# Optimization experiments

Measured on AMD Instinct MI355X. Metric: run time of the kernel, lower is better.

Reference implementation:

```python
import jax, jax.numpy as jnp
import numpy as np

B, N, D, H = 8, 1024, 768, 12
DH = D // H
DFF = 4 * D
EPS = 1e-5


def setup_inputs() -> dict:
    key = jax.random.key(0)
    ks = jax.random.split(key, 16)
    s = 0.02
    return {
        "x": jax.random.normal(ks[0], (B, N, D), jnp.float32),
        "ln1_g": jnp.ones((D,), jnp.float32),
        "ln1_b": jnp.zeros((D,), jnp.float32),
        "wqkv": jax.random.normal(ks[1], (D, 3 * D), jnp.float32) * s,
        "bqkv": jnp.zeros((3 * D,), jnp.float32),
        "wo": jax.random.normal(ks[2], (D, D), jnp.float32) * s,
        "bo": jnp.zeros((D,), jnp.float32),
        "rel_bias": jax.random.normal(ks[3], (H, N, N), jnp.float32) * s,
        "ln2_g": jnp.ones((D,), jnp.float32),
        "ln2_b": jnp.zeros((D,), jnp.float32),
        "w1": jax.random.normal(ks[4], (D, DFF), jnp.float32) * s,
        "b1": jnp.zeros((DFF,), jnp.float32),
        "w2": jax.random.normal(ks[5], (DFF, D), jnp.float32) * s,
        "b2": jnp.zeros((D,), jnp.float32),
    }


def _layer_norm(x, g, b):
    mu = jnp.mean(x, axis=-1, keepdims=True)
    var = jnp.mean(jnp.square(x - mu), axis=-1, keepdims=True)
    return (x - mu) * jax.lax.rsqrt(var + EPS) * g + b


def reference(x, ln1_g, ln1_b, wqkv, bqkv, wo, bo, rel_bias, ln2_g, ln2_b, w1, b1, w2, b2):
    # --- pre-norm self-attention with relative position bias + residual ---
    h = _layer_norm(x, ln1_g, ln1_b)
    qkv = h @ wqkv + bqkv                      # [B, N, 3D]
    qkv = qkv.reshape(B, N, 3, H, DH)
    q, k, v = qkv[:, :, 0], qkv[:, :, 1], qkv[:, :, 2]  # each [B, N, H, DH]
    scale = 1.0 / jnp.sqrt(jnp.asarray(DH, x.dtype))
    scores = jnp.einsum("bnhd,bmhd->bhnm", q, k) * scale + rel_bias[None]
    attn = jax.nn.softmax(scores, axis=-1)
    ctx = jnp.einsum("bhnm,bmhd->bnhd", attn, v).reshape(B, N, D)
    x = ctx @ wo + bo + x
    # --- pre-norm FFN (GELU) + residual ---
    h = _layer_norm(x, ln2_g, ln2_b)
    h = jax.nn.gelu(h @ w1 + b1)
    x = h @ w2 + b2 + x
    return x
```

## Files before the change

### kernel.cpp

```cpp
#include <hip/hip_runtime.h>
#include <hip/hip_bf16.h>
#include <math.h>

#define D_MODEL 768
#define NTOK    8192
#define SEQ     1024
#define NH      12
#define DHD     64
#define DFF     3072

typedef __attribute__((ext_vector_type(8)))  __bf16 bf16x8;
typedef __attribute__((ext_vector_type(4)))  float  f32x4;
typedef __attribute__((ext_vector_type(16))) float  f32x16;
typedef __attribute__((ext_vector_type(4)))  unsigned short us4;

typedef const __attribute__((address_space(1))) void g_void;
typedef __attribute__((address_space(3))) void lds_void;

__device__ __forceinline__ unsigned short f2bf(float f) {
  unsigned u = __float_as_uint(f);
  u += 0x7fffu + ((u >> 16) & 1u);
  return (unsigned short)(u >> 16);
}

__device__ __forceinline__ f32x4 mfma16(bf16x8 a, bf16x8 b, f32x4 c) {
  return __builtin_amdgcn_mfma_f32_16x16x32_bf16(a, b, c, 0, 0, 0);
}
__device__ __forceinline__ f32x16 mfma32(bf16x8 a, bf16x8 b, f32x16 c) {
  return __builtin_amdgcn_mfma_f32_32x32x16_bf16(a, b, c, 0, 0, 0);
}

__device__ __forceinline__ void gload_lds16(const unsigned short* g, unsigned short* l) {
  __builtin_amdgcn_global_load_lds((g_void*)g, (lds_void*)l, 16, 0, 0);
}

__global__ __launch_bounds__(256)
void ln_kernel(const float* __restrict__ x, const float* __restrict__ gam,
               const float* __restrict__ bet, unsigned short* __restrict__ out) {
  const int w = threadIdx.x >> 6, lane = threadIdx.x & 63;
  const size_t row = (size_t)blockIdx.x * 4 + w;
  const float* xr = x + row * D_MODEL;
  f32x4 v[3];
#pragma unroll
  for (int c = 0; c < 3; ++c) v[c] = *(const f32x4*)(xr + c * 256 + lane * 4);
  float s = 0.f;
#pragma unroll
  for (int c = 0; c < 3; ++c)
#pragma unroll
    for (int j = 0; j < 4; ++j) s += v[c][j];
#pragma unroll
  for (int o = 32; o; o >>= 1) s += __shfl_xor(s, o);
  const float mu = s * (1.0f / D_MODEL);
  float vs = 0.f;
#pragma unroll
  for (int c = 0; c < 3; ++c)
#pragma unroll
    for (int j = 0; j < 4; ++j) { float d = v[c][j] - mu; vs += d * d; }
#pragma unroll
  for (int o = 32; o; o >>= 1) vs += __shfl_xor(vs, o);
  const float rs = rsqrtf(vs * (1.0f / D_MODEL) + 1e-5f);
  unsigned short* orow = out + row * D_MODEL;
#pragma unroll
  for (int c = 0; c < 3; ++c) {
    us4 o4;
#pragma unroll
    for (int j = 0; j < 4; ++j) {
      int idx = c * 256 + lane * 4 + j;
      o4[j] = f2bf((v[c][j] - mu) * rs * gam[idx] + bet[idx]);
    }
    *(us4*)(orow + c * 256 + lane * 4) = o4;
  }
}

__global__ __launch_bounds__(256)
void wtrans_kernel(const float* __restrict__ W, unsigned short* __restrict__ Wt,
                   int K, int Nc) {
  __shared__ float t[32][33];
  const int tx = threadIdx.x & 31, ty = threadIdx.x >> 5;
  const int nb = blockIdx.x * 32, kb = blockIdx.y * 32;
#pragma unroll
  for (int i = 0; i < 4; ++i)
    t[ty + 8 * i][tx] = W[(size_t)(kb + ty + 8 * i) * Nc + nb + tx];
  __syncthreads();
#pragma unroll
  for (int i = 0; i < 4; ++i)
    Wt[(size_t)(nb + ty + 8 * i) * K + kb + tx] = f2bf(t[tx][ty + 8 * i]);
}

__global__ __launch_bounds__(256)
void brelayout_kernel(const float* __restrict__ rel, unsigned short* __restrict__ bF) {
  const int gw = blockIdx.x * 4 + (threadIdx.x >> 6);
  const int lane = threadIdx.x & 63;
  const int ktg = gw & 31, qt = (gw >> 5) & 31, h = gw >> 10;
  const int q = qt * 32 + (lane & 31), hi = lane >> 5;
  const float* src = rel + ((size_t)h * SEQ + q) * SEQ + ktg * 32 + 4 * hi;
  unsigned ow[8];
#pragma unroll
  for (int g = 0; g < 4; ++g) {
    f32x4 v = *(const f32x4*)(src + g * 8);
    asm("v_cvt_pk_bf16_f32 %0, %1, %2" : "=v"(ow[2 * g])     : "v"(v[0]), "v"(v[1]));
    asm("v_cvt_pk_bf16_f32 %0, %1, %2" : "=v"(ow[2 * g + 1]) : "v"(v[2]), "v"(v[3]));
  }
  unsigned short* dst = bF + (((size_t)gw) * 64 + lane) * 16;
  *(uint4*)(dst)     = make_uint4(ow[0], ow[1], ow[2], ow[3]);
  *(uint4*)(dst + 8) = make_uint4(ow[4], ow[5], ow[6], ow[7]);
}

#define MODE_QKV  0
#define MODE_PROJ 1
#define MODE_FFN1 2
#define MODE_FFN2 3

template <int MODE>
__global__ __launch_bounds__(256)
void gemm_bt(const unsigned short* __restrict__ A, const unsigned short* __restrict__ Bt,
             int K, const float* __restrict__ bias, const float* __restrict__ resid,
             float* __restrict__ outF, unsigned short* __restrict__ o0,
             unsigned short* __restrict__ o1, unsigned short* __restrict__ o2) {
  __shared__ alignas(16) unsigned short smem[2][2][128 * 64];
  const int tid = threadIdx.x;
  const int w = tid >> 6, lane = tid & 63;
  const int l31 = lane & 31, hi = lane >> 5;
  const int wm = w >> 1, wn = w & 1;
  const int nwg = gridDim.x * gridDim.y;
  const int bid0 = blockIdx.y * gridDim.x + blockIdx.x;
  const int cpx = nwg >> 3;
  const int bid = (bid0 & 7) * cpx + (bid0 >> 3);
  const int bx = bid % gridDim.x, by = bid / gridDim.x;
  const size_t m0 = (size_t)by * 128;
  const size_t n0 = (size_t)bx * 128;
  const unsigned short* gA = A + m0 * K;
  const unsigned short* gB = Bt + n0 * K;

  const int r8 = lane >> 3;
  const int u8 = lane & 7;
  const int ucol = (u8 ^ r8) * 8;

  f32x16 acc[2][2];
#pragma unroll
  for (int i = 0; i < 2; ++i)
#pragma unroll
    for (int j = 0; j < 2; ++j) acc[i][j] = (f32x16)(0.f);
  const int nk = K >> 6;

  auto stage = [&](int buf, int kt) {
#pragma unroll
    for (int g = 0; g < 4; ++g) {
      const int rowb = w * 32 + g * 8;
      gload_lds16(gA + (size_t)(rowb + r8) * K + kt * 64 + ucol, &smem[0][buf][rowb * 64]);
      gload_lds16(gB + (size_t)(rowb + r8) * K + kt * 64 + ucol, &smem[1][buf][rowb * 64]);
    }
  };

  const int swr = l31 & 7;
  const int rA = (wm * 64 + l31) * 64;
  const int rB = (wn * 64 + l31) * 64;

  stage(0, 0);
  __syncthreads();
  for (int kt = 0; kt < nk; ++kt) {
    const int buf = kt & 1;
    if (kt + 1 < nk) stage(buf ^ 1, kt + 1);
    bf16x8 af[2][4], bf[2][4];
#pragma unroll
    for (int mt = 0; mt < 2; ++mt)
#pragma unroll
      for (int ks = 0; ks < 4; ++ks) {
        af[mt][ks] = *(const bf16x8*)&smem[0][buf][rA + mt * 2048 + (((ks * 2 + hi) ^ swr) * 8)];
        bf[mt][ks] = *(const bf16x8*)&smem[1][buf][rB + mt * 2048 + (((ks * 2 + hi) ^ swr) * 8)];
      }
#pragma unroll
    for (int mt = 0; mt < 2; ++mt)
#pragma unroll
      for (int nt = 0; nt < 2; ++nt)
#pragma unroll
        for (int ks = 0; ks < 4; ++ks)
          acc[mt][nt] = mfma32(af[mt][ks], bf[nt][ks], acc[mt][nt]);
    __syncthreads();
  }

  if constexpr (MODE == MODE_QKV) {
    if (bx >= 12) {
      unsigned short* tb = &smem[0][0][0];
#pragma unroll
      for (int mt = 0; mt < 2; ++mt)
#pragma unroll
        for (int nt = 0; nt < 2; ++nt)
#pragma unroll
          for (int r = 0; r < 16; ++r) {
            const int nl = wn * 64 + nt * 32 + l31;
            const int ml = wm * 64 + mt * 32 + (r & 3) + 8 * (r >> 2) + 4 * hi;
            tb[nl * 136 + ml] = f2bf(acc[mt][nt][r] + bias[(int)n0 + nl]);
          }
      __syncthreads();
      const int rr = tid & 127, half = tid >> 7;
      const int n2 = ((int)n0 - 1536) + rr;
      const int hh = n2 >> 6, dh = n2 & 63;
      const int b2 = (int)(m0 >> 10), nq0 = (int)(m0 & 1023);
      unsigned short* dst = o2 + ((size_t)(b2 * NH + hh) * DHD + dh) * SEQ + nq0 + half * 64;
      const unsigned short* src = tb + rr * 136 + half * 64;
#pragma unroll
      for (int i = 0; i < 4; ++i)
        *(uint4*)(dst + i * 8) = *(const uint4*)(src + i * 8);
      return;
    }
  }

#pragma unroll
  for (int mt = 0; mt < 2; ++mt) {
#pragma unroll
    for (int nt = 0; nt < 2; ++nt) {
#pragma unroll
      for (int r = 0; r < 16; ++r) {
        const int m = (int)m0 + wm * 64 + mt * 32 + (r & 3) + 8 * (r >> 2) + 4 * hi;
        const int n = (int)n0 + wn * 64 + nt * 32 + l31;
        float v = acc[mt][nt][r] + bias[n];
        if constexpr (MODE == MODE_QKV) {
          const int b = m >> 10, nq = m & 1023;
          if (n < 768) {
            const int h = n >> 6, dh = n & 63;
            o0[(((size_t)(b * NH + h)) * SEQ + nq) * DHD + dh] = f2bf(v);
          } else {
            const int n2 = n - 768, h = n2 >> 6, dh = n2 & 63;
            o1[(((size_t)(b * NH + h)) * SEQ + nq) * DHD + dh] = f2bf(v);
          }
        } else if constexpr (MODE == MODE_PROJ) {
          const size_t off = (size_t)m * D_MODEL + n;
          outF[off] = v + resid[off];
        } else if constexpr (MODE == MODE_FFN1) {
          const float e = __expf(-1.5957691216057308f * (v + 0.044715f * v * v * v));
          o0[(size_t)m * DFF + n] = f2bf(v / (1.0f + e));
        } else {
          const size_t off = (size_t)m * D_MODEL + n;
          outF[off] = v + resid[off];
        }
      }
    }
  }
}

__global__ __launch_bounds__(256, 3)
void attn_kernel(const unsigned short* __restrict__ q, const unsigned short* __restrict__ k,
                 const unsigned short* __restrict__ vt, const unsigned short* __restrict__ bF,
                 unsigned short* __restrict__ ctx) {
  __shared__ alignas(16) unsigned short kv[2][16][64 * 8];
  constexpr int PSTR = 76;
  __shared__ alignas(16) unsigned short pbuf[4][32 * PSTR];
  const int tid = threadIdx.x, w = tid >> 6, lane = tid & 63;
  const int l31 = lane & 31, hi = lane >> 5;
  const int bid = (blockIdx.x & 7) * 96 + (blockIdx.x >> 3);
  const int bh = bid >> 3, qblk = bid & 7;
  const int b = bh / NH, h = bh % NH;
  const int q0w = qblk * 128 + w * 32;
  const unsigned short* qp = q + (size_t)bh * SEQ * DHD;
  const unsigned short* kp = k + (size_t)bh * SEQ * DHD;
  const unsigned short* vp = vt + (size_t)bh * DHD * SEQ;
  const unsigned short* bfp = bF + ((((size_t)(h * 32 + qblk * 4 + w)) * 32) * 64 + lane) * 16;

  bf16x8 Qf[4];
#pragma unroll
  for (int ds = 0; ds < 4; ++ds)
    Qf[ds] = *(const bf16x8*)(qp + (size_t)(q0w + l31) * DHD + ds * 16 + hi * 8);

  f32x16 o[2];
#pragma unroll
  for (int dt = 0; dt < 2; ++dt) o[dt] = (f32x16)(0.f);
  float mrun = -INFINITY, lrun = 0.f;
  const float scale = 0.125f;
  unsigned short* pw = pbuf[w];

  auto stage = [&](int buf, int kb) {
    if (w < 2) {
      const unsigned short* g0 = kp + (size_t)(kb * 64 + w * 32 + l31) * DHD + hi * 8;
#pragma unroll
      for (int ds = 0; ds < 4; ++ds)
        gload_lds16(g0 + ds * 16, &kv[buf][w * 4 + ds][0]);
    } else {
      const int dt = w - 2;
      const unsigned short* g0 = vp + (size_t)(dt * 32 + l31) * SEQ + kb * 64 + hi * 8;
#pragma unroll
      for (int kh = 0; kh < 4; ++kh)
        gload_lds16(g0 + kh * 16, &kv[buf][8 + dt * 4 + kh][0]);
    }
  };

  stage(0, 0);
  __syncthreads();
  for (int kb = 0; kb < SEQ / 64; ++kb) {
    const int buf = kb & 1;
    if (kb + 1 < SEQ / 64) stage(buf ^ 1, kb + 1);

    f32x16 s0 = (f32x16)(0.f), s1 = (f32x16)(0.f);
    __builtin_amdgcn_s_setprio(1);
#pragma unroll
    for (int ds = 0; ds < 4; ++ds) {
      bf16x8 kf0 = *(const bf16x8*)&kv[buf][ds][lane * 8];
      s0 = mfma32(kf0, Qf[ds], s0);
      bf16x8 kf1 = *(const bf16x8*)&kv[buf][4 + ds][lane * 8];
      s1 = mfma32(kf1, Qf[ds], s1);
    }
    __builtin_amdgcn_s_setprio(0);

    const unsigned short* bb = bfp + (size_t)(kb * 2) * 64 * 16;
    uint4 a0 = *(const uint4*)(bb),            a1 = *(const uint4*)(bb + 8);
    uint4 c0 = *(const uint4*)(bb + 64 * 16),  c1 = *(const uint4*)(bb + 64 * 16 + 8);
    unsigned uw0[8] = {a0.x, a0.y, a0.z, a0.w, a1.x, a1.y, a1.z, a1.w};
    unsigned uw1[8] = {c0.x, c0.y, c0.z, c0.w, c1.x, c1.y, c1.z, c1.w};
    float p0[16], p1[16];
#pragma unroll
    for (int j = 0; j < 8; ++j) {
      p0[2 * j]     = fmaf(s0[2 * j],     scale, __uint_as_float(uw0[j] << 16));
      p0[2 * j + 1] = fmaf(s0[2 * j + 1], scale, __uint_as_float(uw0[j] & 0xffff0000u));
      p1[2 * j]     = fmaf(s1[2 * j],     scale, __uint_as_float(uw1[j] << 16));
      p1[2 * j + 1] = fmaf(s1[2 * j + 1], scale, __uint_as_float(uw1[j] & 0xffff0000u));
    }

    float pmax = p0[0];
#pragma unroll
    for (int i = 1; i < 16; ++i) pmax = fmaxf(pmax, p0[i]);
#pragma unroll
    for (int i = 0; i < 16; ++i) pmax = fmaxf(pmax, p1[i]);
    if (!__all(pmax - mrun <= 8.0f)) {
      float pm = fmaxf(pmax, __shfl_xor(pmax, 32));
      const float mn = fmaxf(mrun, pm);
      const float al = __expf(mrun - mn);
      mrun = mn;
      lrun *= al;
#pragma unroll
      for (int dt = 0; dt < 2; ++dt)
#pragma unroll
        for (int r = 0; r < 16; ++r) o[dt][r] *= al;
    }
#pragma unroll
    for (int i = 0; i < 16; ++i) { p0[i] = __expf(p0[i] - mrun); lrun += p0[i]; }
#pragma unroll
    for (int i = 0; i < 16; ++i) { p1[i] = __expf(p1[i] - mrun); lrun += p1[i]; }

#pragma unroll
    for (int g = 0; g < 4; ++g) {
      uint2 w0, w1;
      asm("v_cvt_pk_bf16_f32 %0, %1, %2" : "=v"(w0.x) : "v"(p0[4 * g]),     "v"(p0[4 * g + 1]));
      asm("v_cvt_pk_bf16_f32 %0, %1, %2" : "=v"(w0.y) : "v"(p0[4 * g + 2]), "v"(p0[4 * g + 3]));
      asm("v_cvt_pk_bf16_f32 %0, %1, %2" : "=v"(w1.x) : "v"(p1[4 * g]),     "v"(p1[4 * g + 1]));
      asm("v_cvt_pk_bf16_f32 %0, %1, %2" : "=v"(w1.y) : "v"(p1[4 * g + 2]), "v"(p1[4 * g + 3]));
      *(uint2*)(pw + l31 * PSTR +      g * 8 + 4 * hi) = w0;
      *(uint2*)(pw + l31 * PSTR + 32 + g * 8 + 4 * hi) = w1;
    }
    bf16x8 pf[4];
#pragma unroll
    for (int kh = 0; kh < 4; ++kh)
      pf[kh] = *(const bf16x8*)(pw + l31 * PSTR + kh * 16 + hi * 8);

    __builtin_amdgcn_s_setprio(1);
#pragma unroll
    for (int dt = 0; dt < 2; ++dt)
#pragma unroll
      for (int kh = 0; kh < 4; ++kh) {
        bf16x8 vf = *(const bf16x8*)&kv[buf][8 + dt * 4 + kh][lane * 8];
        o[dt] = mfma32(vf, pf[kh], o[dt]);
      }
    __builtin_amdgcn_s_setprio(0);

    __syncthreads();
  }

  lrun += __shfl_xor(lrun, 32);
  const float inv = 1.0f / lrun;
  unsigned short* crow = ctx + ((size_t)b * SEQ + q0w + l31) * D_MODEL + h * DHD;
#pragma unroll
  for (int dt = 0; dt < 2; ++dt)
#pragma unroll
    for (int g = 0; g < 4; ++g) {
      us4 ov;
#pragma unroll
      for (int j = 0; j < 4; ++j) ov[j] = f2bf(o[dt][4 * g + j] * inv);
      *(us4*)(crow + dt * 32 + g * 8 + 4 * hi) = ov;
    }
}

extern "C" void kernel_launch(void* const* d_in, const int* in_sizes, int n_in,
                              void* d_out, int out_size, void* d_ws, size_t ws_size,
                              hipStream_t stream) {
  (void)in_sizes; (void)n_in; (void)out_size; (void)ws_size;
  const float* x     = (const float*)d_in[0];
  const float* ln1_g = (const float*)d_in[1];
  const float* ln1_b = (const float*)d_in[2];
  const float* wqkv  = (const float*)d_in[3];
  const float* bqkv  = (const float*)d_in[4];
  const float* wo    = (const float*)d_in[5];
  const float* bo    = (const float*)d_in[6];
  const float* rel   = (const float*)d_in[7];
  const float* ln2_g = (const float*)d_in[8];
  const float* ln2_b = (const float*)d_in[9];
  const float* w1    = (const float*)d_in[10];
  const float* b1    = (const float*)d_in[11];
  const float* w2    = (const float*)d_in[12];
  const float* b2    = (const float*)d_in[13];
  float* out = (float*)d_out;

  char* p = (char*)d_ws;
  auto take = [&](size_t bytes) {
    void* r = (void*)p;
    p += (bytes + 255) & ~(size_t)255;
    return r;
  };
  unsigned short* hbuf  = (unsigned short*)take((size_t)NTOK * D_MODEL * 2);
  unsigned short* wqkvT = (unsigned short*)take((size_t)2304 * 768 * 2);
  unsigned short* woT   = (unsigned short*)take((size_t)768 * 768 * 2);
  unsigned short* w1T   = (unsigned short*)take((size_t)3072 * 768 * 2);
  unsigned short* w2T   = (unsigned short*)take((size_t)768 * 3072 * 2);
  unsigned short* qbuf  = (unsigned short*)take((size_t)8 * NH * SEQ * DHD * 2);
  unsigned short* kbuf  = (unsigned short*)take((size_t)8 * NH * SEQ * DHD * 2);
  unsigned short* vtbuf = (unsigned short*)take((size_t)8 * NH * SEQ * DHD * 2);
  unsigned short* ctxb  = (unsigned short*)take((size_t)NTOK * D_MODEL * 2);
  unsigned short* h1buf = (unsigned short*)take((size_t)NTOK * DFF * 2);
  unsigned short* biasF = h1buf;

  wtrans_kernel<<<dim3(2304 / 32, 768 / 32), 256, 0, stream>>>(wqkv, wqkvT, 768, 2304);
  wtrans_kernel<<<dim3(768 / 32, 768 / 32), 256, 0, stream>>>(wo, woT, 768, 768);
  wtrans_kernel<<<dim3(3072 / 32, 768 / 32), 256, 0, stream>>>(w1, w1T, 768, 3072);
  wtrans_kernel<<<dim3(768 / 32, 3072 / 32), 256, 0, stream>>>(w2, w2T, 3072, 768);
  brelayout_kernel<<<NH * 32 * 32 / 4, 256, 0, stream>>>(rel, biasF);

  ln_kernel<<<NTOK / 4, 256, 0, stream>>>(x, ln1_g, ln1_b, hbuf);
  gemm_bt<MODE_QKV><<<dim3(2304 / 128, NTOK / 128), 256, 0, stream>>>(
      hbuf, wqkvT, 768, bqkv, nullptr, nullptr, qbuf, kbuf, vtbuf);
  attn_kernel<<<8 * NH * (SEQ / 128), 256, 0, stream>>>(qbuf, kbuf, vtbuf, biasF, ctxb);
  gemm_bt<MODE_PROJ><<<dim3(768 / 128, NTOK / 128), 256, 0, stream>>>(
      ctxb, woT, 768, bo, x, out, nullptr, nullptr, nullptr);
  ln_kernel<<<NTOK / 4, 256, 0, stream>>>(out, ln2_g, ln2_b, hbuf);
  gemm_bt<MODE_FFN1><<<dim3(DFF / 128, NTOK / 128), 256, 0, stream>>>(
      hbuf, w1T, 768, b1, nullptr, nullptr, h1buf, nullptr, nullptr);
  gemm_bt<MODE_FFN2><<<dim3(768 / 128, NTOK / 128), 256, 0, stream>>>(
      h1buf, w2T, 3072, b2, out, out, nullptr, nullptr, nullptr);
}
```

Measured before the change: 284.4 us.

## Use exp2 softmax with folded scale and permlane swap instead of LDS P roundtrip

Folds the 1/sqrt(dh)*log2(e) factor into Q at the QKV GEMM epilogue and log2(e) into the relative bias relayout, so the attention inner loop uses a plain add and native exp2. It replaces the per-wave LDS write/read of the probability tile with v_permlane32_swap register shuffles that build the MFMA B operands directly. Removing the pbuf LDS allocation lets the launch bounds target 4 blocks per SM, and the lazy-rescale threshold is widened to match the log2 domain. Risks include slight precision changes from bf16-rounding the prescaled Q and bias, and register pressure at the higher occupancy target.

```diff
diff --git a/kernel.cpp b/kernel.cpp
--- a/kernel.cpp
+++ b/kernel.cpp
@@ -32,6 +32,15 @@
 
 __device__ __forceinline__ void gload_lds16(const unsigned short* g, unsigned short* l) {
   __builtin_amdgcn_global_load_lds((g_void*)g, (lds_void*)l, 16, 0, 0);
+}
+
+__device__ __forceinline__ void plswap(unsigned &a, unsigned &b) {
+  asm("v_permlane32_swap_b32 %0, %1" : "+v"(a), "+v"(b));
+}
+__device__ __forceinline__ bf16x8 mk8(unsigned a, unsigned b, unsigned c, unsigned d) {
+  union { unsigned u[4]; bf16x8 v; } t;
+  t.u[0] = a; t.u[1] = b; t.u[2] = c; t.u[3] = d;
+  return t.v;
 }
 
 __global__ __launch_bounds__(256)
@@ -94,12 +103,13 @@
   const int ktg = gw & 31, qt = (gw >> 5) & 31, h = gw >> 10;
   const int q = qt * 32 + (lane & 31), hi = lane >> 5;
   const float* src = rel + ((size_t)h * SEQ + q) * SEQ + ktg * 32 + 4 * hi;
+  const float L2E = 1.4426950408889634f;
   unsigned ow[8];
 #pragma unroll
   for (int g = 0; g < 4; ++g) {
     f32x4 v = *(const f32x4*)(src + g * 8);
-    asm("v_cvt_pk_bf16_f32 %0, %1, %2" : "=v"(ow[2 * g])     : "v"(v[0]), "v"(v[1]));
-    asm("v_cvt_pk_bf16_f32 %0, %1, %2" : "=v"(ow[2 * g + 1]) : "v"(v[2]), "v"(v[3]));
+    asm("v_cvt_pk_bf16_f32 %0, %1, %2" : "=v"(ow[2 * g])     : "v"(v[0] * L2E), "v"(v[1] * L2E));
+    asm("v_cvt_pk_bf16_f32 %0, %1, %2" : "=v"(ow[2 * g + 1]) : "v"(v[2] * L2E), "v"(v[3] * L2E));
   }
   unsigned short* dst = bF + (((size_t)gw) * 64 + lane) * 16;
   *(uint4*)(dst)     = make_uint4(ow[0], ow[1], ow[2], ow[3]);
@@ -219,7 +229,8 @@
           const int b = m >> 10, nq = m & 1023;
           if (n < 768) {
             const int h = n >> 6, dh = n & 63;
-            o0[(((size_t)(b * NH + h)) * SEQ + nq) * DHD + dh] = f2bf(v);
+            o0[(((size_t)(b * NH + h)) * SEQ + nq) * DHD + dh] =
+                f2bf(v * 0.1803368801111244f);
           } else {
             const int n2 = n - 768, h = n2 >> 6, dh = n2 & 63;
             o1[(((size_t)(b * NH + h)) * SEQ + nq) * DHD + dh] = f2bf(v);
@@ -239,13 +250,11 @@
   }
 }
 
-__global__ __launch_bounds__(256, 3)
+__global__ __launch_bounds__(256, 4)
 void attn_kernel(const unsigned short* __restrict__ q, const unsigned short* __restrict__ k,
                  const unsigned short* __restrict__ vt, const unsigned short* __restrict__ bF,
                  unsigned short* __restrict__ ctx) {
   __shared__ alignas(16) unsigned short kv[2][16][64 * 8];
-  constexpr int PSTR = 76;
-  __shared__ alignas(16) unsigned short pbuf[4][32 * PSTR];
   const int tid = threadIdx.x, w = tid >> 6, lane = tid & 63;
   const int l31 = lane & 31, hi = lane >> 5;
   const int bid = (blockIdx.x & 7) * 96 + (blockIdx.x >> 3);
@@ -266,8 +275,6 @@
 #pragma unroll
   for (int dt = 0; dt < 2; ++dt) o[dt] = (f32x16)(0.f);
   float mrun = -INFINITY, lrun = 0.f;
-  const float scale = 0.125f;
-  unsigned short* pw = pbuf[w];
 
   auto stage = [&](int buf, int kb) {
     if (w < 2) {
@@ -309,10 +316,10 @@
     float p0[16], p1[16];
 #pragma unroll
     for (int j = 0; j < 8; ++j) {
-      p0[2 * j]     = fmaf(s0[2 * j],     scale, __uint_as_float(uw0[j] << 16));
-      p0[2 * j + 1] = fmaf(s0[2 * j + 1], scale, __uint_as_float(uw0[j] & 0xffff0000u));
-      p1[2 * j]     = fmaf(s1[2 * j],     scale, __uint_as_float(uw1[j] << 16));
-      p1[2 * j + 1] = fmaf(s1[2 * j + 1], scale, __uint_as_float(uw1[j] & 0xffff0000u));
+      p0[2 * j]     = s0[2 * j]     + __uint_as_float(uw0[j] << 16);
+      p0[2 * j + 1] = s0[2 * j + 1] + __uint_as_float(uw0[j] & 0xffff0000u);
+      p1[2 * j]     = s1[2 * j]     + __uint_as_float(uw1[j] << 16);
+      p1[2 * j + 1] = s1[2 * j + 1] + __uint_as_float(uw1[j] & 0xffff0000u);
     }
 
     float pmax = p0[0];
@@ -320,10 +327,10 @@
     for (int i = 1; i < 16; ++i) pmax = fmaxf(pmax, p0[i]);
 #pragma unroll
     for (int i = 0; i < 16; ++i) pmax = fmaxf(pmax, p1[i]);
-    if (!__all(pmax - mrun <= 8.0f)) {
+    if (!__all(pmax - mrun <= 11.0f)) {
       float pm = fmaxf(pmax, __shfl_xor(pmax, 32));
       const float mn = fmaxf(mrun, pm);
-      const float al = __expf(mrun - mn);
+      const float al = __builtin_amdgcn_exp2f(mrun - mn);
       mrun = mn;
       lrun *= al;
 #pragma unroll
@@ -332,24 +339,25 @@
         for (int r = 0; r < 16; ++r) o[dt][r] *= al;
     }
 #pragma unroll
-    for (int i = 0; i < 16; ++i) { p0[i] = __expf(p0[i] - mrun); lrun += p0[i]; }
-#pragma unroll
-    for (int i = 0; i < 16; ++i) { p1[i] = __expf(p1[i] - mrun); lrun += p1[i]; }
-
-#pragma unroll
-    for (int g = 0; g < 4; ++g) {
-      uint2 w0, w1;
-      asm("v_cvt_pk_bf16_f32 %0, %1, %2" : "=v"(w0.x) : "v"(p0[4 * g]),     "v"(p0[4 * g + 1]));
-      asm("v_cvt_pk_bf16_f32 %0, %1, %2" : "=v"(w0.y) : "v"(p0[4 * g + 2]), "v"(p0[4 * g + 3]));
-      asm("v_cvt_pk_bf16_f32 %0, %1, %2" : "=v"(w1.x) : "v"(p1[4 * g]),     "v"(p1[4 * g + 1]));
-      asm("v_cvt_pk_bf16_f32 %0, %1, %2" : "=v"(w1.y) : "v"(p1[4 * g + 2]), "v"(p1[4 * g + 3]));
-      *(uint2*)(pw + l31 * PSTR +      g * 8 + 4 * hi) = w0;
-      *(uint2*)(pw + l31 * PSTR + 32 + g * 8 + 4 * hi) = w1;
-    }
+    for (int i = 0; i < 16; ++i) { p0[i] = __builtin_amdgcn_exp2f(p0[i] - mrun); lrun += p0[i]; }
+#pragma unroll
+    for (int i = 0; i < 16; ++i) { p1[i] = __builtin_amdgcn_exp2f(p1[i] - mrun); lrun += p1[i]; }
+
+    unsigned wpk[16];
+#pragma unroll
+    for (int i = 0; i < 8; ++i) {
+      asm("v_cvt_pk_bf16_f32 %0, %1, %2" : "=v"(wpk[i])     : "v"(p0[2 * i]), "v"(p0[2 * i + 1]));
+      asm("v_cvt_pk_bf16_f32 %0, %1, %2" : "=v"(wpk[8 + i]) : "v"(p1[2 * i]), "v"(p1[2 * i + 1]));
+    }
+    plswap(wpk[0], wpk[2]);   plswap(wpk[1], wpk[3]);
+    plswap(wpk[4], wpk[6]);   plswap(wpk[5], wpk[7]);
+    plswap(wpk[8], wpk[10]);  plswap(wpk[9], wpk[11]);
+    plswap(wpk[12], wpk[14]); plswap(wpk[13], wpk[15]);
     bf16x8 pf[4];
-#pragma unroll
-    for (int kh = 0; kh < 4; ++kh)
-      pf[kh] = *(const bf16x8*)(pw + l31 * PSTR + kh * 16 + hi * 8);
+    pf[0] = mk8(wpk[0], wpk[1], wpk[2], wpk[3]);
+    pf[1] = mk8(wpk[4], wpk[5], wpk[6], wpk[7]);
+    pf[2] = mk8(wpk[8], wpk[9], wpk[10], wpk[11]);
+    pf[3] = mk8(wpk[12], wpk[13], wpk[14], wpk[15]);
 
     __builtin_amdgcn_s_setprio(1);
 #pragma unroll
```

New measurement: 274.8 us. 1.03x faster.
